# Performance work log

Measured on AMD Instinct MI355X. Metric: run time of the kernel, lower is better.

Reference implementation:

```python
import jax, jax.numpy as jnp
import numpy as np

EMBED_DIM = 384
HEADS = 6
HEAD_DIM = EMBED_DIM // HEADS
WINDOW = 64


def setup_inputs() -> dict:
    key = jax.random.key(0)
    ks = jax.random.split(key, 5)
    B, T = 128, 256
    s_attn = 1.0 / np.sqrt(EMBED_DIM)
    x = jax.random.normal(ks[0], (B, T, EMBED_DIM), dtype=jnp.float32)
    W_attn = jax.random.normal(ks[1], (EMBED_DIM, 3 * EMBED_DIM), dtype=jnp.float32) * s_attn
    b_attn = jax.random.normal(ks[2], (3 * EMBED_DIM,), dtype=jnp.float32) * 0.02
    W_proj = jax.random.normal(ks[3], (EMBED_DIM, EMBED_DIM), dtype=jnp.float32) * s_attn
    b_proj = jax.random.normal(ks[4], (EMBED_DIM,), dtype=jnp.float32) * 0.02
    return {"x": x, "W_attn": W_attn, "b_attn": b_attn, "W_proj": W_proj, "b_proj": b_proj}


def reference(x, W_attn, b_attn, W_proj, b_proj):
    B, T, C = x.shape
    qkv = x @ W_attn + b_attn  # [B,T,3C]
    q, k, v = jnp.split(qkv, 3, axis=-1)
    # [B, H, T, hd]
    q = q.reshape(B, T, HEADS, HEAD_DIM).transpose(0, 2, 1, 3)
    k = k.reshape(B, T, HEADS, HEAD_DIM).transpose(0, 2, 1, 3)
    v = v.reshape(B, T, HEADS, HEAD_DIM).transpose(0, 2, 1, 3)
    scale = 1.0 / np.sqrt(HEAD_DIM).astype(np.float32)
    att = jnp.einsum('bhqd,bhkd->bhqk', q, k) * scale
    i = jnp.arange(T)
    causal = i[:, None] >= i[None, :]
    local = jnp.abs(i[:, None] - i[None, :]) <= WINDOW
    mask = (causal & local)[None, None, :, :]
    att = jnp.where(mask, att, -jnp.inf)
    att = jax.nn.softmax(att, axis=-1)
    y = jnp.einsum('bhqk,bhkd->bhqd', att, v)
    y = y.transpose(0, 2, 1, 3).reshape(B, T, C)
    return y @ W_proj + b_proj
```

## Files before the change

### kernel.cpp

```cpp
#include <hip/hip_runtime.h>

#define B_SZ   128
#define T_SEQ  256
#define C_DIM  384
#define HEADS  6
#define HD     64
#define WIN    64

typedef __bf16 bf16x8 __attribute__((ext_vector_type(8)));
typedef float  f32x4  __attribute__((ext_vector_type(4)));

typedef __attribute__((address_space(3))) void lds_void;
typedef __attribute__((address_space(1))) void gbl_void;

__device__ __forceinline__ unsigned short f2bf(float f) {
  unsigned u = __float_as_uint(f);
  u += 0x7FFFu + ((u >> 16) & 1u);
  return (unsigned short)(u >> 16);
}

__global__ __launch_bounds__(256) void convert_f32_bf16(
    const float* __restrict__ in, unsigned short* __restrict__ out, int n4) {
  int i = blockIdx.x * blockDim.x + threadIdx.x;
  if (i < n4) {
    float4 v = ((const float4*)in)[i];
    ushort4 o;
    o.x = f2bf(v.x); o.y = f2bf(v.y); o.z = f2bf(v.z); o.w = f2bf(v.w);
    ((ushort4*)out)[i] = o;
  }
}

__global__ __launch_bounds__(256) void transpose_convert(
    const float* __restrict__ in, unsigned short* __restrict__ out,
    int K, int N) {
  __shared__ float tile[32][33];
  const int gx = blockIdx.x * 32;
  const int gy = blockIdx.y * 32;
  const int tx = threadIdx.x;
  const int ty = threadIdx.y;
#pragma unroll
  for (int r = ty; r < 32; r += 8)
    tile[r][tx] = in[(size_t)(gy + r) * N + gx + tx];
  __syncthreads();
#pragma unroll
  for (int r = ty; r < 32; r += 8)
    out[(size_t)(gx + r) * K + gy + tx] = f2bf(tile[tx][r]);
}

template <bool OUT_BF16>
__global__ __launch_bounds__(256, 4) void gemm_mfma_bf16(
    const unsigned short* __restrict__ A,
    const unsigned short* __restrict__ Bt,
    const float* __restrict__ bias,
    void* __restrict__ Cv, int M, int N, int K, int tiles_n) {
  __shared__ __attribute__((aligned(16))) char smem_raw[64 * 132 * 4];
  unsigned short* As0 = (unsigned short*)smem_raw;
  unsigned short* Bs0 = As0 + 128 * 32;
  unsigned short* As1 = Bs0 + 128 * 32;
  unsigned short* Bs1 = As1 + 128 * 32;
  float* ep = (float*)smem_raw;

  const int t    = threadIdx.x;
  const int lane = t & 63;
  const int w    = t >> 6;
  const int wr   = w >> 1;
  const int wc   = w & 1;

  const unsigned id    = blockIdx.x;
  const unsigned remap = (id & 7u) * (gridDim.x >> 3) + (id >> 3);
  const int by = remap / (unsigned)tiles_n;
  const int bx = remap % (unsigned)tiles_n;
  const int m0 = by * 128;
  const int n0 = bx * 128;

  const int lrow = lane >> 2;
  const int lcol = lane & 3;
  const int sc   = lcol ^ ((lrow >> 1) & 3);

  const int m16  = lane & 15;
  const int quad = lane >> 4;
  const int cp   = (quad ^ ((m16 >> 1) & 3)) << 3;

  f32x4 acc[4][4];
#pragma unroll
  for (int i = 0; i < 4; ++i)
#pragma unroll
    for (int j = 0; j < 4; ++j) acc[i][j] = (f32x4){0.f, 0.f, 0.f, 0.f};

  auto stage = [&](unsigned short* Ad, unsigned short* Bd, int k0) {
#pragma unroll
    for (int i = 0; i < 2; ++i) {
      const int inst = w * 2 + i;
      const int r = inst * 16 + lrow;
      const unsigned short* ga = A + (size_t)(m0 + r) * K + k0 + sc * 8;
      __builtin_amdgcn_global_load_lds((const gbl_void*)ga,
                                       (lds_void*)(Ad + inst * 512), 16, 0, 0);
    }
#pragma unroll
    for (int i = 0; i < 2; ++i) {
      const int inst = w * 2 + i;
      const int r = inst * 16 + lrow;
      const unsigned short* gb = Bt + (size_t)(n0 + r) * K + k0 + sc * 8;
      __builtin_amdgcn_global_load_lds((const gbl_void*)gb,
                                       (lds_void*)(Bd + inst * 512), 16, 0, 0);
    }
  };

  const int nk = K >> 5;
  stage(As0, Bs0, 0);
  __syncthreads();

  unsigned short *Ac = As0, *Bc = Bs0, *An = As1, *Bn = Bs1;
  for (int kt = 0; kt < nk; ++kt) {
    if (kt + 1 < nk) stage(An, Bn, (kt + 1) << 5);

    bf16x8 af[4];
#pragma unroll
    for (int mt = 0; mt < 4; ++mt)
      af[mt] = *(const bf16x8*)(Ac + (size_t)(wr * 64 + mt * 16 + m16) * 32 + cp);
#pragma unroll
    for (int nt = 0; nt < 4; ++nt) {
      bf16x8 bfr = *(const bf16x8*)(Bc + (size_t)(wc * 64 + nt * 16 + m16) * 32 + cp);
#pragma unroll
      for (int mt = 0; mt < 4; ++mt)
        acc[mt][nt] = __builtin_amdgcn_mfma_f32_16x16x32_bf16(
            af[mt], bfr, acc[mt][nt], 0, 0, 0);
    }
    __syncthreads();
    unsigned short* tp;
    tp = Ac; Ac = An; An = tp;
    tp = Bc; Bc = Bn; Bn = tp;
  }

  float bv[4];
#pragma unroll
  for (int nt = 0; nt < 4; ++nt) bv[nt] = bias[n0 + wc * 64 + nt * 16 + m16];

#pragma unroll
  for (int p = 0; p < 2; ++p) {
    if (p) __syncthreads();
    if (wr == p) {
#pragma unroll
      for (int mt = 0; mt < 4; ++mt)
#pragma unroll
        for (int nt = 0; nt < 4; ++nt)
#pragma unroll
          for (int r = 0; r < 4; ++r)
            ep[(mt * 16 + quad * 4 + r) * 132 + wc * 64 + nt * 16 + m16] =
                acc[mt][nt][r] + bv[nt];
    }
    __syncthreads();
#pragma unroll
    for (int cc = 0; cc < 8; ++cc) {
      const int chunk = cc * 256 + t;
      const int row = chunk >> 5;
      const int c4  = chunk & 31;
      f32x4 v = *(const f32x4*)(ep + row * 132 + c4 * 4);
      const int grow = m0 + p * 64 + row;
      const int gcol = n0 + c4 * 4;
      if (OUT_BF16) {
        ushort4 o;
        o.x = f2bf(v[0]); o.y = f2bf(v[1]); o.z = f2bf(v[2]); o.w = f2bf(v[3]);
        *(ushort4*)((unsigned short*)Cv + (size_t)grow * N + gcol) = o;
      } else {
        *(f32x4*)((float*)Cv + (size_t)grow * N + gcol) = v;
      }
    }
  }
}

#define PSTR 68
__global__ __launch_bounds__(256) void attn_mfma(
    const unsigned short* __restrict__ qkv, unsigned short* __restrict__ y) {
  __shared__ unsigned short Qs[64 * 64];
  __shared__ unsigned short Ks[64 * 64];
  __shared__ unsigned short Vt[64 * 64];
  __shared__ float Pw[4][16 * PSTR];

  const unsigned id  = blockIdx.x;
  const unsigned bid = (id & 7u) * (gridDim.x >> 3) + (id >> 3);
  const int qt  = bid & 3;
  const int h   = (bid >> 2) % HEADS;
  const int b   = bid / (4 * HEADS);
  const int t   = threadIdx.x;
  const int lane = t & 63;
  const int w    = t >> 6;
  const int quad = lane >> 4;
  const int m16  = lane & 15;
  const int sw   = m16 & 7;

  const size_t rowbase = (size_t)b * T_SEQ * (3 * C_DIM);
  const int qoff = h * HD;
  const int koff = C_DIM + h * HD;
  const int voff = 2 * C_DIM + h * HD;
  const int qg0  = qt * 64;

  const int lrow = lane >> 3;
  const int lcol = lane & 7;
  const int schunk = lcol ^ lrow;

#pragma unroll
  for (int i = 0; i < 2; ++i) {
    const int inst = w * 2 + i;
    const int r = inst * 8 + lrow;
    const unsigned short* ga =
        qkv + rowbase + (size_t)(qg0 + r) * (3 * C_DIM) + qoff + schunk * 8;
    __builtin_amdgcn_global_load_lds((const gbl_void*)ga,
                                     (lds_void*)(Qs + inst * 512), 16, 0, 0);
  }

  float m_r[4], l_r[4];
  f32x4 yacc[4];
#pragma unroll
  for (int r = 0; r < 4; ++r) { m_r[r] = -1e30f; l_r[r] = 0.f; }
#pragma unroll
  for (int dt = 0; dt < 4; ++dt) yacc[dt] = (f32x4){0.f, 0.f, 0.f, 0.f};

  const int nchunks  = (qt == 0) ? 1 : 2;
  const int kb_first = (qt == 0) ? 0 : (qg0 - 64);
  const int qrow_base = qg0 + w * 16 + quad * 4;

  for (int ch = 0; ch < nchunks; ++ch) {
    const int kb = kb_first + ch * 64;

    __syncthreads();

#pragma unroll
    for (int i = 0; i < 2; ++i) {
      const int inst = w * 2 + i;
      const int r = inst * 8 + lrow;
      const unsigned short* ga =
          qkv + rowbase + (size_t)(kb + r) * (3 * C_DIM) + koff + schunk * 8;
      __builtin_amdgcn_global_load_lds((const gbl_void*)ga,
                                       (lds_void*)(Ks + inst * 512), 16, 0, 0);
    }
    {
      const int vkey = t & 63;
      const int kc = vkey >> 3, ke = vkey & 7;
      const int vd0  = (t >> 6) * 16;
      const unsigned short* gv =
          qkv + rowbase + (size_t)(kb + vkey) * (3 * C_DIM) + voff + vd0;
#pragma unroll
      for (int u = 0; u < 4; ++u) {
        ushort4 vv = *(const ushort4*)(gv + u * 4);
#pragma unroll
        for (int jj = 0; jj < 4; ++jj) {
          const int d = vd0 + u * 4 + jj;
          const unsigned short val =
              (jj == 0) ? vv.x : (jj == 1) ? vv.y : (jj == 2) ? vv.z : vv.w;
          Vt[d * 64 + ((kc ^ (d & 7)) << 3) + ke] = val;
        }
      }
    }
    __syncthreads();

    f32x4 sacc[4];
#pragma unroll
    for (int nt = 0; nt < 4; ++nt) sacc[nt] = (f32x4){0.f, 0.f, 0.f, 0.f};
#pragma unroll
    for (int ks = 0; ks < 64; ks += 32) {
      const int cp = (((ks >> 3) + quad) ^ sw) << 3;
      bf16x8 aq = *(const bf16x8*)(Qs + (size_t)(w * 16 + m16) * 64 + cp);
#pragma unroll
      for (int nt = 0; nt < 4; ++nt) {
        bf16x8 kf = *(const bf16x8*)(Ks + (size_t)(nt * 16 + m16) * 64 + cp);
        sacc[nt] = __builtin_amdgcn_mfma_f32_16x16x32_bf16(aq, kf, sacc[nt], 0, 0, 0);
      }
    }

    float mc[4] = {-1e30f, -1e30f, -1e30f, -1e30f};
#pragma unroll
    for (int nt = 0; nt < 4; ++nt) {
      const int kg = kb + nt * 16 + m16;
#pragma unroll
      for (int r = 0; r < 4; ++r) {
        const int qg = qrow_base + r;
        const bool valid = (kg <= qg) && (qg - kg <= WIN);
        const float sv = valid ? (sacc[nt][r] * 0.125f) : -1e30f;
        sacc[nt][r] = sv;
        mc[r] = fmaxf(mc[r], sv);
      }
    }
#pragma unroll
    for (int r = 0; r < 4; ++r) {
#pragma unroll
      for (int x = 1; x <= 8; x <<= 1) mc[r] = fmaxf(mc[r], __shfl_xor(mc[r], x));
    }

#pragma unroll
    for (int r = 0; r < 4; ++r) {
      const float mn    = fmaxf(m_r[r], mc[r]);
      const float alpha = __expf(m_r[r] - mn);
      m_r[r] = mn;
      l_r[r] *= alpha;
#pragma unroll
      for (int dt = 0; dt < 4; ++dt) yacc[dt][r] *= alpha;
      float ls = 0.f;
#pragma unroll
      for (int nt = 0; nt < 4; ++nt) {
        const float p = __expf(sacc[nt][r] - mn);
        sacc[nt][r] = p;
        ls += p;
      }
#pragma unroll
      for (int x = 1; x <= 8; x <<= 1) ls += __shfl_xor(ls, x);
      l_r[r] += ls;
    }

#pragma unroll
    for (int nt = 0; nt < 4; ++nt)
#pragma unroll
      for (int r = 0; r < 4; ++r)
        Pw[w][(quad * 4 + r) * PSTR + nt * 16 + m16] = sacc[nt][r];

#pragma unroll
    for (int ks = 0; ks < 64; ks += 32) {
      f32x4 pa = *(const f32x4*)(&Pw[w][m16 * PSTR + ks + quad * 8]);
      f32x4 pb = *(const f32x4*)(&Pw[w][m16 * PSTR + ks + quad * 8 + 4]);
      bf16x8 ap;
#pragma unroll
      for (int j = 0; j < 4; ++j) {
        ap[j]     = (__bf16)pa[j];
        ap[4 + j] = (__bf16)pb[j];
      }
      const int cp = (((ks >> 3) + quad) ^ sw) << 3;
#pragma unroll
      for (int dt = 0; dt < 4; ++dt) {
        bf16x8 vf = *(const bf16x8*)(Vt + (size_t)(dt * 16 + m16) * 64 + cp);
        yacc[dt] = __builtin_amdgcn_mfma_f32_16x16x32_bf16(ap, vf, yacc[dt], 0, 0, 0);
      }
    }
  }

  float* epy = &Pw[0][0];
  float inv[4];
#pragma unroll
  for (int r = 0; r < 4; ++r) inv[r] = 1.f / l_r[r];
#pragma unroll
  for (int dt = 0; dt < 4; ++dt)
#pragma unroll
    for (int r = 0; r < 4; ++r)
      epy[(w * 16 + quad * 4 + r) * PSTR + dt * 16 + m16] = yacc[dt][r] * inv[r];
  __syncthreads();
#pragma unroll
  for (int cc = 0; cc < 4; ++cc) {
    const int chunk = cc * 256 + t;
    const int row = chunk >> 4;
    const int c4  = chunk & 15;
    f32x4 v = *(const f32x4*)(epy + row * PSTR + c4 * 4);
    ushort4 o;
    o.x = f2bf(v[0]); o.y = f2bf(v[1]); o.z = f2bf(v[2]); o.w = f2bf(v[3]);
    *(ushort4*)(y + (size_t)(b * T_SEQ + qg0 + row) * C_DIM + h * HD + c4 * 4) = o;
  }
}

extern "C" void kernel_launch(void* const* d_in, const int* in_sizes, int n_in,
                              void* d_out, int out_size, void* d_ws, size_t ws_size,
                              hipStream_t stream) {
  const float* x      = (const float*)d_in[0];
  const float* W_attn = (const float*)d_in[1];
  const float* b_attn = (const float*)d_in[2];
  const float* W_proj = (const float*)d_in[3];
  const float* b_proj = (const float*)d_in[4];
  float* out = (float*)d_out;

  const int M = B_SZ * T_SEQ;

  unsigned short* qkv_b = (unsigned short*)d_ws;
  unsigned short* y_b   = qkv_b + (size_t)M * (3 * C_DIM);
  unsigned short* x_b   = y_b   + (size_t)M * C_DIM;
  unsigned short* Wa_t  = x_b   + (size_t)M * C_DIM;
  unsigned short* Wp_t  = Wa_t  + (size_t)(3 * C_DIM) * C_DIM;

  {
    int n4 = M * C_DIM / 4;
    convert_f32_bf16<<<n4 / 256, 256, 0, stream>>>(x, x_b, n4);
    transpose_convert<<<dim3((3 * C_DIM) / 32, C_DIM / 32), dim3(32, 8), 0, stream>>>(
        W_attn, Wa_t, C_DIM, 3 * C_DIM);
    transpose_convert<<<dim3(C_DIM / 32, C_DIM / 32), dim3(32, 8), 0, stream>>>(
        W_proj, Wp_t, C_DIM, C_DIM);
  }

  gemm_mfma_bf16<true><<<dim3(9 * (M / 128)), 256, 0, stream>>>(
      x_b, Wa_t, b_attn, qkv_b, M, 3 * C_DIM, C_DIM, 9);

  attn_mfma<<<dim3(B_SZ * HEADS * (T_SEQ / 64)), 256, 0, stream>>>(qkv_b, y_b);

  gemm_mfma_bf16<false><<<dim3(3 * (M / 128)), 256, 0, stream>>>(
      y_b, Wp_t, b_proj, out, M, C_DIM, C_DIM, 3);
}
```

Baseline: 202.4 us.

## Triple-buffer GEMM LDS staging with vmcnt waits and compile-time K

Replaces the double-buffered global-to-LDS pipeline in the bf16 MFMA GEMM with a three-slot ring that keeps two k-tiles in flight. It uses explicit s_waitcnt vmcnt plus a single barrier per iteration, so the trailing barrier after each compute step goes away. K becomes a template parameter so the loop can be fully unrolled. The price is 48KB of LDS instead of about 33KB and a launch-bounds hint lowered from 4 to 3, which may cut occupancy.

```diff
diff --git a/kernel.cpp b/kernel.cpp
--- a/kernel.cpp
+++ b/kernel.cpp
@@ -47,18 +47,16 @@
     out[(size_t)(gx + r) * K + gy + tx] = f2bf(tile[tx][r]);
 }
 
-template <bool OUT_BF16>
-__global__ __launch_bounds__(256, 4) void gemm_mfma_bf16(
+template <bool OUT_BF16, int KK>
+__global__ __launch_bounds__(256, 3) void gemm_mfma_bf16(
     const unsigned short* __restrict__ A,
     const unsigned short* __restrict__ Bt,
     const float* __restrict__ bias,
-    void* __restrict__ Cv, int M, int N, int K, int tiles_n) {
-  __shared__ __attribute__((aligned(16))) char smem_raw[64 * 132 * 4];
-  unsigned short* As0 = (unsigned short*)smem_raw;
-  unsigned short* Bs0 = As0 + 128 * 32;
-  unsigned short* As1 = Bs0 + 128 * 32;
-  unsigned short* Bs1 = As1 + 128 * 32;
+    void* __restrict__ Cv, int M, int N, int tiles_n) {
+  __shared__ __attribute__((aligned(16))) char smem_raw[49152];
   float* ep = (float*)smem_raw;
+
+  constexpr int NK = KK / 32;
 
   const int t    = threadIdx.x;
   const int lane = t & 63;
@@ -87,12 +85,14 @@
 #pragma unroll
     for (int j = 0; j < 4; ++j) acc[i][j] = (f32x4){0.f, 0.f, 0.f, 0.f};
 
-  auto stage = [&](unsigned short* Ad, unsigned short* Bd, int k0) {
+  auto stage = [&](int slot, int k0) {
+    unsigned short* Ad = (unsigned short*)(smem_raw + slot * 16384);
+    unsigned short* Bd = Ad + 128 * 32;
 #pragma unroll
     for (int i = 0; i < 2; ++i) {
       const int inst = w * 2 + i;
       const int r = inst * 16 + lrow;
-      const unsigned short* ga = A + (size_t)(m0 + r) * K + k0 + sc * 8;
+      const unsigned short* ga = A + (size_t)(m0 + r) * KK + k0 + sc * 8;
       __builtin_amdgcn_global_load_lds((const gbl_void*)ga,
                                        (lds_void*)(Ad + inst * 512), 16, 0, 0);
     }
@@ -100,19 +100,29 @@
     for (int i = 0; i < 2; ++i) {
       const int inst = w * 2 + i;
       const int r = inst * 16 + lrow;
-      const unsigned short* gb = Bt + (size_t)(n0 + r) * K + k0 + sc * 8;
+      const unsigned short* gb = Bt + (size_t)(n0 + r) * KK + k0 + sc * 8;
       __builtin_amdgcn_global_load_lds((const gbl_void*)gb,
                                        (lds_void*)(Bd + inst * 512), 16, 0, 0);
     }
   };
 
-  const int nk = K >> 5;
-  stage(As0, Bs0, 0);
-  __syncthreads();
-
-  unsigned short *Ac = As0, *Bc = Bs0, *An = As1, *Bn = Bs1;
-  for (int kt = 0; kt < nk; ++kt) {
-    if (kt + 1 < nk) stage(An, Bn, (kt + 1) << 5);
+  stage(0, 0);
+  stage(1, 32);
+
+#pragma unroll
+  for (int kt = 0; kt < NK; ++kt) {
+    if (kt + 1 < NK)
+      asm volatile("s_waitcnt vmcnt(4)" ::: "memory");
+    else
+      asm volatile("s_waitcnt vmcnt(0)" ::: "memory");
+    __builtin_amdgcn_s_barrier();
+    __builtin_amdgcn_sched_barrier(0);
+
+    if (kt + 2 < NK) stage((kt + 2) % 3, (kt + 2) * 32);
+
+    const unsigned short* Ac =
+        (const unsigned short*)(smem_raw + (kt % 3) * 16384);
+    const unsigned short* Bc = Ac + 128 * 32;
 
     bf16x8 af[4];
 #pragma unroll
@@ -126,11 +136,8 @@
         acc[mt][nt] = __builtin_amdgcn_mfma_f32_16x16x32_bf16(
             af[mt], bfr, acc[mt][nt], 0, 0, 0);
     }
-    __syncthreads();
-    unsigned short* tp;
-    tp = Ac; Ac = An; An = tp;
-    tp = Bc; Bc = Bn; Bn = tp;
-  }
+  }
+  __syncthreads();
 
   float bv[4];
 #pragma unroll
@@ -381,11 +388,11 @@
         W_proj, Wp_t, C_DIM, C_DIM);
   }
 
-  gemm_mfma_bf16<true><<<dim3(9 * (M / 128)), 256, 0, stream>>>(
-      x_b, Wa_t, b_attn, qkv_b, M, 3 * C_DIM, C_DIM, 9);
+  gemm_mfma_bf16<true, C_DIM><<<dim3(9 * (M / 128)), 256, 0, stream>>>(
+      x_b, Wa_t, b_attn, qkv_b, M, 3 * C_DIM, 9);
 
   attn_mfma<<<dim3(B_SZ * HEADS * (T_SEQ / 64)), 256, 0, stream>>>(qkv_b, y_b);
 
-  gemm_mfma_bf16<false><<<dim3(3 * (M / 128)), 256, 0, stream>>>(
-      y_b, Wp_t, b_proj, out, M, C_DIM, C_DIM, 3);
-}
+  gemm_mfma_bf16<false, C_DIM><<<dim3(3 * (M / 128)), 256, 0, stream>>>(
+      y_b, Wp_t, b_proj, out, M, C_DIM, 3);
+}
```

New measurement: 201.7 us. Within noise of the previous version (-0.3%).
